# Kernel optimization log

Hardware: AMD Instinct MI355X
Metric: run time of the kernel (lower is better)

Reference implementation:

```python
import jax, jax.numpy as jnp
import numpy as np

NUM_BLOCKS_PER_ROW = 64
NUM_BLOCKS_PER_COLUMN = 36
N = NUM_BLOCKS_PER_ROW * NUM_BLOCKS_PER_COLUMN  # 2304 nodes per frame
F = 32   # frames in the GOP (linear reference chain)
B = 1024  # batch = number of candidate anchor points
S = 256   # selected anchor points


def setup_inputs() -> dict:
    key = jax.random.key(0)
    k1, k2, k3, k4 = jax.random.split(key, 4)
    # weights[f] propagates cumulated error from frame f -> frame f+1; scaled small
    # so the 31-step propagation chain stays numerically tame.
    weights = jax.random.normal(k1, (F - 1, N, N), dtype=jnp.float32) * 0.02
    biases = jax.random.uniform(k2, (F, N), dtype=jnp.float32)  # per-frame tc bias
    selected_anchor_points = jax.random.randint(k3, (S, 3), 0, 32, dtype=jnp.int32)
    candidate_anchor_points = jax.random.randint(k4, (B, 3), 0, 32, dtype=jnp.int32)
    return {
        "weights": weights,
        "biases": biases,
        "selected_anchor_points": selected_anchor_points,
        "candidate_anchor_points": candidate_anchor_points,
    }


def _forward(weights, biases, selected_anchor_points, candidate_anchor_points):
    dtype = biases.dtype
    # flatten (row, col) -> node index, same as row * num_blocks_per_row + col
    sel_f = selected_anchor_points[:, 0]
    sel_node = selected_anchor_points[:, 1] * NUM_BLOCKS_PER_ROW + selected_anchor_points[:, 2]
    cand_f = candidate_anchor_points[:, 0]
    cand_node = candidate_anchor_points[:, 1] * NUM_BLOCKS_PER_ROW + candidate_anchor_points[:, 2]

    # selected anchors zero a node's column for ALL batch rows in their frame
    keep_sel = jnp.ones((F, N), dtype=dtype).at[sel_f, sel_node].set(0.0)  # [F, N]
    # candidate anchors zero one (batch, node) entry in their frame
    cand_oh = jax.nn.one_hot(cand_node, N, dtype=dtype)  # [B, N]

    def apply_masks(err, f):
        # err: [B, N] cumulated error of frame f
        err = err * keep_sel[f][None, :]
        kill = (cand_f == f).astype(dtype)[:, None] * cand_oh  # [B, N]
        return err * (1.0 - kill)

    # root (key) frame: bias only
    err0 = apply_masks(jnp.broadcast_to(biases[0], (B, N)), 0)
    total0 = jnp.sum(err0, axis=1)  # [B]

    def step(carry, xs):
        prev_err, total = carry
        w_f, b_f, f = xs
        # torch.sparse.mm(W, prev.T).T == prev @ W.T
        cur = b_f[None, :] + jnp.matmul(prev_err, w_f.T)  # [B, N]
        cur = apply_masks(cur, f)
        return (cur, total + jnp.sum(cur, axis=1)), None

    frame_ids = jnp.arange(1, F)
    (_, total), _ = jax.lax.scan(step, (err0, total0), (weights, biases[1:], frame_ids))
    return total  # [B] per-candidate summed error


def reference(weights, biases, selected_anchor_points, candidate_anchor_points):
    return _forward(weights, biases, selected_anchor_points, candidate_anchor_points)
```

## Files before the change

kernel.cpp:

```cpp
#include <hip/hip_runtime.h>
#include <stdint.h>

#define NN 2304
#define NF 32
#define NB 1024
#define NS 256

#define BM 128
#define BN 96
#define BK 64
#define KSLICES (NN / BK)
#define DEPTH 4
#define NBUF 5
#define NGRP 8
#define GRPBLKS 24

typedef short bf16x8 __attribute__((ext_vector_type(8)));
typedef float f32x4  __attribute__((ext_vector_type(4)));

__device__ __forceinline__ unsigned short f2bf(float f) {
  union { float f; unsigned u; } v; v.f = f;
  return (unsigned short)((v.u + 0x7FFFu + ((v.u >> 16) & 1u)) >> 16);
}

__device__ __forceinline__ void async16(const void* g, void* l) {
  __builtin_amdgcn_global_load_lds((const __attribute__((address_space(1))) void*)g,
                                   (__attribute__((address_space(3))) void*)l, 16, 0, 0);
}

#define WAITV(n) asm volatile("s_waitcnt vmcnt(" #n ")" ::: "memory")

__global__ void convert_w(const f32x4* __restrict__ W4, bf16x8* __restrict__ Wb8) {
  const int total = (31 * NN * NN) / 8;
  for (int gid = blockIdx.x * 256 + threadIdx.x; gid < total; gid += gridDim.x * 256) {
    f32x4 x = W4[2 * gid], y = W4[2 * gid + 1];
    bf16x8 o;
    o[0] = (short)f2bf(x[0]); o[1] = (short)f2bf(x[1]);
    o[2] = (short)f2bf(x[2]); o[3] = (short)f2bf(x[3]);
    o[4] = (short)f2bf(y[0]); o[5] = (short)f2bf(y[1]);
    o[6] = (short)f2bf(y[2]); o[7] = (short)f2bf(y[3]);
    Wb8[gid] = o;
  }
}

__global__ void build_masks(const int* __restrict__ cand, float* __restrict__ keep,
                            int* __restrict__ cf, int* __restrict__ cn,
                            float* __restrict__ out, int* __restrict__ bar) {
  int gid = blockIdx.x * 256 + threadIdx.x;
  if (gid < NF * NN) keep[gid] = 1.0f;
  if (gid < NB) {
    cf[gid] = cand[3 * gid];
    cn[gid] = cand[3 * gid + 1] * 64 + cand[3 * gid + 2];
    out[gid] = 0.f;
  }
  if (gid < NGRP * NF) bar[gid] = 0;
}

__global__ void scatter_sel(const int* __restrict__ sel, float* __restrict__ keep) {
  int s = threadIdx.x;
  int sf = sel[3 * s], sn = sel[3 * s + 1] * 64 + sel[3 * s + 2];
  keep[sf * NN + sn] = 0.0f;
}

__device__ __forceinline__ void group_barrier(int* cnt, int t) {
  __syncthreads();
  if (t == 0) {
    __builtin_amdgcn_fence(__ATOMIC_RELEASE, "agent");
    __hip_atomic_fetch_add(cnt, 1, __ATOMIC_RELAXED, __HIP_MEMORY_SCOPE_AGENT);
    while (__hip_atomic_load(cnt, __ATOMIC_RELAXED, __HIP_MEMORY_SCOPE_AGENT) < GRPBLKS)
      __builtin_amdgcn_s_sleep(2);
    __builtin_amdgcn_fence(__ATOMIC_ACQUIRE, "agent");
  }
  __syncthreads();
}

__launch_bounds__(512, 2)
__global__ void persist_kernel(const unsigned short* __restrict__ Wb,
                               const float* __restrict__ biases,
                               const float* __restrict__ keep,
                               const int* __restrict__ cf, const int* __restrict__ cn,
                               unsigned short* __restrict__ errA,
                               unsigned short* __restrict__ errB,
                               float* __restrict__ out, int* __restrict__ bar) {
  __shared__ __align__(16) unsigned char sA[NBUF][BM * BK * 2];
  __shared__ __align__(16) unsigned char sB[NBUF][BN * BK * 2];

  const int t = threadIdx.x;
  const int l = t & 63, w = t >> 6;
  const int wm = w >> 1, wn = w & 1;
  const int id = blockIdx.x;
  const int g = id & 7;
  const int mBase = g * BM;
  const int nBase = (id >> 3) * BN;

  {
    const int row = mBase + (t >> 2);
    const int c0 = nBase + (t & 3) * 24;
    const int kn = (cf[row] == 0) ? cn[row] : -1;
    float sum = 0.f;
    for (int j = 0; j < 24; ++j) {
      const int col = c0 + j;
      float v = biases[col] * keep[col];
      if (col == kn) v = 0.f;
      errA[row * NN + col] = f2bf(v);
      sum += v;
    }
    sum += __shfl_xor(sum, 1, 64);
    sum += __shfl_xor(sum, 2, 64);
    if ((t & 3) == 0) atomicAdd(&out[row], sum);
  }
  group_barrier(&bar[g * NF + 0], t);

  const int sRow = l >> 3;
  const int sCk = (l & 7) ^ sRow;
  const bool aRole = (w < 4);
  const int rw = aRole ? w : (w - 4);
  const int ldsOff = aRole ? (rw * 32 * 128 + l * 16) : (rw * 24 * 128 + l * 16);
  const int gRowOff = aRole ? ((mBase + rw * 32 + sRow) * NN + sCk * 8)
                            : ((nBase + rw * 24 + sRow) * NN + sCk * 8);

  const int fl = l & 15, q = l >> 4;
  const int fragB0 = (q ^ (fl & 7)) * 16;

  for (int f = 1; f < NF; ++f) {
    const unsigned short* Ain = (f & 1) ? errA : errB;
    unsigned short* errOut = (f & 1) ? errB : errA;
    const unsigned short* gSrc =
        (aRole ? Ain : Wb + (size_t)(f - 1) * NN * NN) + gRowOff;
    const float* biasf = biases + f * NN;
    const float* keepf = keep + f * NN;

    f32x4 acc[2][3];
#pragma unroll
    for (int r = 0; r < 2; ++r)
#pragma unroll
      for (int c = 0; c < 3; ++c) acc[r][c] = (f32x4){0.f, 0.f, 0.f, 0.f};

#pragma unroll
    for (int p = 0; p < DEPTH; ++p) {
      const unsigned short* gp = gSrc + p * BK;
      if (aRole) {
        unsigned char* la = &sA[p][ldsOff];
#pragma unroll
        for (int c = 0; c < 4; ++c) async16(gp + c * 8 * NN, la + c * 8 * 128);
      } else {
        unsigned char* lb = &sB[p][ldsOff];
#pragma unroll
        for (int c = 0; c < 3; ++c) async16(gp + c * 8 * NN, lb + c * 8 * 128);
      }
    }

    int rbuf = 0, wbuf = DEPTH;
    for (int s = 0; s < KSLICES; ++s) {
      const int ahead = KSLICES - 1 - s;
      if (ahead >= 3) { if (aRole) WAITV(12); else WAITV(9); }
      else if (ahead == 2) { if (aRole) WAITV(8); else WAITV(6); }
      else if (ahead == 1) { if (aRole) WAITV(4); else WAITV(3); }
      else { WAITV(0); }
      asm volatile("s_barrier" ::: "memory");
      if (s + DEPTH < KSLICES) {
        const unsigned short* gp = gSrc + (s + DEPTH) * BK;
        if (aRole) {
          unsigned char* la = &sA[wbuf][ldsOff];
#pragma unroll
          for (int c = 0; c < 4; ++c) async16(gp + c * 8 * NN, la + c * 8 * 128);
        } else {
          unsigned char* lb = &sB[wbuf][ldsOff];
#pragma unroll
          for (int c = 0; c < 3; ++c) async16(gp + c * 8 * NN, lb + c * 8 * 128);
        }
      }

      const unsigned char* pa = &sA[rbuf][(wm * 32 + fl) * 128];
      const unsigned char* pb = &sB[rbuf][(wn * 48 + fl) * 128];
      __builtin_amdgcn_s_setprio(1);
#pragma unroll
      for (int h = 0; h < 2; ++h) {
        const int cb = fragB0 ^ (h * 64);
        bf16x8 aF[2], bF[3];
#pragma unroll
        for (int r = 0; r < 2; ++r) aF[r] = *(const bf16x8*)(pa + r * 2048 + cb);
#pragma unroll
        for (int c = 0; c < 3; ++c) bF[c] = *(const bf16x8*)(pb + c * 2048 + cb);
#pragma unroll
        for (int r = 0; r < 2; ++r)
#pragma unroll
          for (int c = 0; c < 3; ++c)
            acc[r][c] = __builtin_amdgcn_mfma_f32_16x16x32_bf16(aF[r], bF[c], acc[r][c], 0, 0, 0);
      }
      __builtin_amdgcn_s_setprio(0);
      rbuf = (rbuf == NBUF - 1) ? 0 : rbuf + 1;
      wbuf = (wbuf == NBUF - 1) ? 0 : wbuf + 1;
    }

#pragma unroll
    for (int r = 0; r < 2; ++r) {
      float rs[4] = {0.f, 0.f, 0.f, 0.f};
      const int rowB = mBase + wm * 32 + r * 16 + q * 4;
#pragma unroll
      for (int c = 0; c < 3; ++c) {
        const int col = nBase + wn * 48 + c * 16 + fl;
        const float kv = keepf[col], bv = biasf[col];
#pragma unroll
        for (int i = 0; i < 4; ++i) {
          const int row = rowB + i;
          float v = (acc[r][c][i] + bv) * kv;
          if (cf[row] == f && cn[row] == col) v = 0.f;
          errOut[row * NN + col] = f2bf(v);
          rs[i] += v;
        }
      }
#pragma unroll
      for (int m = 1; m < 16; m <<= 1) {
#pragma unroll
        for (int i = 0; i < 4; ++i) rs[i] += __shfl_xor(rs[i], m, 64);
      }
      if (fl == 0) {
#pragma unroll
        for (int i = 0; i < 4; ++i) atomicAdd(&out[rowB + i], rs[i]);
      }
    }

    group_barrier(&bar[g * NF + f], t);
  }
}

extern "C" void kernel_launch(void* const* d_in, const int* in_sizes, int n_in,
                              void* d_out, int out_size, void* d_ws, size_t ws_size,
                              hipStream_t stream) {
  (void)in_sizes; (void)n_in; (void)out_size; (void)ws_size;
  const float* W = (const float*)d_in[0];
  const float* biases = (const float*)d_in[1];
  const int* sel = (const int*)d_in[2];
  const int* cand = (const int*)d_in[3];
  float* out = (float*)d_out;
  char* ws = (char*)d_ws;

  size_t off = 0;
  unsigned short* Wb = (unsigned short*)(ws + off); off += (size_t)31 * NN * NN * 2;
  float* keep = (float*)(ws + off); off += (size_t)NF * NN * 4;
  int* cf = (int*)(ws + off); off += NB * 4;
  int* cn = (int*)(ws + off); off += NB * 4;
  int* bar = (int*)(ws + off); off += NGRP * NF * 4;
  off = (off + 255) & ~(size_t)255;
  unsigned short* errA = (unsigned short*)(ws + off); off += (size_t)NB * NN * 2;
  unsigned short* errB = (unsigned short*)(ws + off);

  convert_w<<<4096, 256, 0, stream>>>((const f32x4*)W, (bf16x8*)Wb);
  build_masks<<<(NF * NN + 255) / 256, 256, 0, stream>>>(cand, keep, cf, cn, out, bar);
  scatter_sel<<<1, NS, 0, stream>>>(sel, keep);

  const unsigned short* WbC = Wb;
  void* kargs[] = {(void*)&WbC, (void*)&biases, (void*)&keep, (void*)&cf, (void*)&cn,
                   (void*)&errA, (void*)&errB, (void*)&out, (void*)&bar};
  hipError_t e = hipLaunchCooperativeKernel(
      reinterpret_cast<void*>(persist_kernel), dim3(NGRP * GRPBLKS), dim3(512),
      kargs, 0, stream);
  if (e != hipSuccess) {
    persist_kernel<<<NGRP * GRPBLKS, 512, 0, stream>>>(Wb, biases, keep, cf, cn,
                                                       errA, errB, out, bar);
  }
}
```

Measured before the change: 1.977 ms.

## Reshape tiles to 256x48 to halve weight re-reads, use global barrier

Changes the block tile from 128x96 to 256x48 so each weight matrix is streamed by only four row-groups instead of eight, reducing weight traffic. All eight warps now load A rows and six warps load B rows, with prefetch depth lowered to three. Synchronization between frames becomes a single global barrier over all 192 blocks instead of per-group barriers, which adds wider sync latency and doubles A-tile loads.

```diff
diff --git a/kernel.cpp b/kernel.cpp
--- a/kernel.cpp
+++ b/kernel.cpp
@@ -6,14 +6,13 @@
 #define NB 1024
 #define NS 256
 
-#define BM 128
-#define BN 96
+#define BM 256
+#define BN 48
 #define BK 64
 #define KSLICES (NN / BK)
-#define DEPTH 4
-#define NBUF 5
-#define NGRP 8
-#define GRPBLKS 24
+#define DEPTH 3
+#define NBUF 4
+#define NBLK 192
 
 typedef short bf16x8 __attribute__((ext_vector_type(8)));
 typedef float f32x4  __attribute__((ext_vector_type(4)));
@@ -53,7 +52,7 @@
     cn[gid] = cand[3 * gid + 1] * 64 + cand[3 * gid + 2];
     out[gid] = 0.f;
   }
-  if (gid < NGRP * NF) bar[gid] = 0;
+  if (gid < NF) bar[gid] = 0;
 }
 
 __global__ void scatter_sel(const int* __restrict__ sel, float* __restrict__ keep) {
@@ -62,12 +61,12 @@
   keep[sf * NN + sn] = 0.0f;
 }
 
-__device__ __forceinline__ void group_barrier(int* cnt, int t) {
+__device__ __forceinline__ void global_barrier(int* cnt, int t) {
   __syncthreads();
   if (t == 0) {
     __builtin_amdgcn_fence(__ATOMIC_RELEASE, "agent");
     __hip_atomic_fetch_add(cnt, 1, __ATOMIC_RELAXED, __HIP_MEMORY_SCOPE_AGENT);
-    while (__hip_atomic_load(cnt, __ATOMIC_RELAXED, __HIP_MEMORY_SCOPE_AGENT) < GRPBLKS)
+    while (__hip_atomic_load(cnt, __ATOMIC_RELAXED, __HIP_MEMORY_SCOPE_AGENT) < NBLK)
       __builtin_amdgcn_s_sleep(2);
     __builtin_amdgcn_fence(__ATOMIC_ACQUIRE, "agent");
   }
@@ -87,15 +86,14 @@
 
   const int t = threadIdx.x;
   const int l = t & 63, w = t >> 6;
-  const int wm = w >> 1, wn = w & 1;
   const int id = blockIdx.x;
-  const int g = id & 7;
+  const int g = id & 3;
   const int mBase = g * BM;
-  const int nBase = (id >> 3) * BN;
+  const int nBase = (id >> 2) * BN;
 
   {
-    const int row = mBase + (t >> 2);
-    const int c0 = nBase + (t & 3) * 24;
+    const int row = mBase + (t >> 1);
+    const int c0 = nBase + (t & 1) * 24;
     const int kn = (cf[row] == 0) ? cn[row] : -1;
     float sum = 0.f;
     for (int j = 0; j < 24; ++j) {
@@ -106,18 +104,17 @@
       sum += v;
     }
     sum += __shfl_xor(sum, 1, 64);
-    sum += __shfl_xor(sum, 2, 64);
-    if ((t & 3) == 0) atomicAdd(&out[row], sum);
-  }
-  group_barrier(&bar[g * NF + 0], t);
+    if ((t & 1) == 0) atomicAdd(&out[row], sum);
+  }
+  global_barrier(&bar[0], t);
 
   const int sRow = l >> 3;
   const int sCk = (l & 7) ^ sRow;
-  const bool aRole = (w < 4);
-  const int rw = aRole ? w : (w - 4);
-  const int ldsOff = aRole ? (rw * 32 * 128 + l * 16) : (rw * 24 * 128 + l * 16);
-  const int gRowOff = aRole ? ((mBase + rw * 32 + sRow) * NN + sCk * 8)
-                            : ((nBase + rw * 24 + sRow) * NN + sCk * 8);
+  const bool bRole = (w < 6);
+  const int gAOff = (mBase + w * 32 + sRow) * NN + sCk * 8;
+  const int gBOff = (nBase + (bRole ? w : 0) * 8 + sRow) * NN + sCk * 8;
+  const int ldsA = w * 32 * 128 + l * 16;
+  const int ldsB = w * 8 * 128 + l * 16;
 
   const int fl = l & 15, q = l >> 4;
   const int fragB0 = (q ^ (fl & 7)) * 16;
@@ -125,8 +122,8 @@
   for (int f = 1; f < NF; ++f) {
     const unsigned short* Ain = (f & 1) ? errA : errB;
     unsigned short* errOut = (f & 1) ? errB : errA;
-    const unsigned short* gSrc =
-        (aRole ? Ain : Wb + (size_t)(f - 1) * NN * NN) + gRowOff;
+    const unsigned short* gA = Ain + gAOff;
+    const unsigned short* gB = Wb + (size_t)(f - 1) * NN * NN + gBOff;
     const float* biasf = biases + f * NN;
     const float* keepf = keep + f * NN;
 
@@ -138,41 +135,30 @@
 
 #pragma unroll
     for (int p = 0; p < DEPTH; ++p) {
-      const unsigned short* gp = gSrc + p * BK;
-      if (aRole) {
-        unsigned char* la = &sA[p][ldsOff];
-#pragma unroll
-        for (int c = 0; c < 4; ++c) async16(gp + c * 8 * NN, la + c * 8 * 128);
-      } else {
-        unsigned char* lb = &sB[p][ldsOff];
-#pragma unroll
-        for (int c = 0; c < 3; ++c) async16(gp + c * 8 * NN, lb + c * 8 * 128);
-      }
+      const unsigned short* ga = gA + p * BK;
+      unsigned char* la = &sA[p][ldsA];
+#pragma unroll
+      for (int c = 0; c < 4; ++c) async16(ga + c * 8 * NN, la + c * 8 * 128);
+      if (bRole) async16(gB + p * BK, &sB[p][ldsB]);
     }
 
     int rbuf = 0, wbuf = DEPTH;
     for (int s = 0; s < KSLICES; ++s) {
       const int ahead = KSLICES - 1 - s;
-      if (ahead >= 3) { if (aRole) WAITV(12); else WAITV(9); }
-      else if (ahead == 2) { if (aRole) WAITV(8); else WAITV(6); }
-      else if (ahead == 1) { if (aRole) WAITV(4); else WAITV(3); }
+      if (ahead >= 2) { if (bRole) WAITV(10); else WAITV(8); }
+      else if (ahead == 1) { if (bRole) WAITV(5); else WAITV(4); }
       else { WAITV(0); }
       asm volatile("s_barrier" ::: "memory");
       if (s + DEPTH < KSLICES) {
-        const unsigned short* gp = gSrc + (s + DEPTH) * BK;
-        if (aRole) {
-          unsigned char* la = &sA[wbuf][ldsOff];
-#pragma unroll
-          for (int c = 0; c < 4; ++c) async16(gp + c * 8 * NN, la + c * 8 * 128);
-        } else {
-          unsigned char* lb = &sB[wbuf][ldsOff];
-#pragma unroll
-          for (int c = 0; c < 3; ++c) async16(gp + c * 8 * NN, lb + c * 8 * 128);
-        }
-      }
-
-      const unsigned char* pa = &sA[rbuf][(wm * 32 + fl) * 128];
-      const unsigned char* pb = &sB[rbuf][(wn * 48 + fl) * 128];
+        const unsigned short* ga = gA + (s + DEPTH) * BK;
+        unsigned char* la = &sA[wbuf][ldsA];
+#pragma unroll
+        for (int c = 0; c < 4; ++c) async16(ga + c * 8 * NN, la + c * 8 * 128);
+        if (bRole) async16(gB + (s + DEPTH) * BK, &sB[wbuf][ldsB]);
+      }
+
+      const unsigned char* pa = &sA[rbuf][(w * 32 + fl) * 128];
+      const unsigned char* pb = &sB[rbuf][fl * 128];
       __builtin_amdgcn_s_setprio(1);
 #pragma unroll
       for (int h = 0; h < 2; ++h) {
@@ -196,10 +182,10 @@
 #pragma unroll
     for (int r = 0; r < 2; ++r) {
       float rs[4] = {0.f, 0.f, 0.f, 0.f};
-      const int rowB = mBase + wm * 32 + r * 16 + q * 4;
+      const int rowB = mBase + w * 32 + r * 16 + q * 4;
 #pragma unroll
       for (int c = 0; c < 3; ++c) {
-        const int col = nBase + wn * 48 + c * 16 + fl;
+        const int col = nBase + c * 16 + fl;
         const float kv = keepf[col], bv = biasf[col];
 #pragma unroll
         for (int i = 0; i < 4; ++i) {
@@ -221,7 +207,7 @@
       }
     }
 
-    group_barrier(&bar[g * NF + f], t);
+    global_barrier(&bar[f], t);
   }
 }
 
@@ -241,7 +227,7 @@
   float* keep = (float*)(ws + off); off += (size_t)NF * NN * 4;
   int* cf = (int*)(ws + off); off += NB * 4;
   int* cn = (int*)(ws + off); off += NB * 4;
-  int* bar = (int*)(ws + off); off += NGRP * NF * 4;
+  int* bar = (int*)(ws + off); off += NF * 4;
   off = (off + 255) & ~(size_t)255;
   unsigned short* errA = (unsigned short*)(ws + off); off += (size_t)NB * NN * 2;
   unsigned short* errB = (unsigned short*)(ws + off);
@@ -254,10 +240,10 @@
   void* kargs[] = {(void*)&WbC, (void*)&biases, (void*)&keep, (void*)&cf, (void*)&cn,
                    (void*)&errA, (void*)&errB, (void*)&out, (void*)&bar};
   hipError_t e = hipLaunchCooperativeKernel(
-      reinterpret_cast<void*>(persist_kernel), dim3(NGRP * GRPBLKS), dim3(512),
+      reinterpret_cast<void*>(persist_kernel), dim3(NBLK), dim3(512),
       kargs, 0, stream);
   if (e != hipSuccess) {
-    persist_kernel<<<NGRP * GRPBLKS, 512, 0, stream>>>(Wb, biases, keep, cf, cn,
-                                                       errA, errB, out, bar);
-  }
-}
+    persist_kernel<<<NBLK, 512, 0, stream>>>(Wb, biases, keep, cf, cn,
+                                             errA, errB, out, bar);
+  }
+}
```

Result: slower. 2.779 ms (+40.6%).
